# Kernel optimization log

Measured on AMD Instinct MI355X. Metric: run time of the kernel, lower is better.

## Reference

```python
import jax, jax.numpy as jnp
import numpy as np

N_NODES = 50000
N_EDGES = 600000
IN_DIM = 128
HID_DIM = 128
OUT_DIM = 128
N_GRAPHS = 64


def _glorot(key, shape):
    lim = np.sqrt(6.0 / (shape[0] + shape[1]))
    return jax.random.uniform(key, shape, jnp.float32, -lim, lim)


def setup_inputs() -> dict:
    key = jax.random.key(0)
    ks = jax.random.split(key, 8)
    h = jax.random.normal(ks[0], (N_NODES, IN_DIM), jnp.float32)
    src = jax.random.randint(ks[1], (N_EDGES,), 0, N_NODES, jnp.int64)
    dst = jax.random.randint(ks[2], (N_EDGES,), 0, N_NODES, jnp.int64)
    graph_ids = jnp.sort(jax.random.randint(ks[3], (N_NODES,), 0, N_GRAPHS, jnp.int64))
    W1 = _glorot(ks[4], (IN_DIM, HID_DIM)); b1 = jnp.zeros((HID_DIM,), jnp.float32)
    W2 = _glorot(ks[5], (HID_DIM, HID_DIM)); b2 = jnp.zeros((HID_DIM,), jnp.float32)
    W3 = _glorot(ks[6], (HID_DIM, OUT_DIM)); b3 = jnp.zeros((OUT_DIM,), jnp.float32)
    return {"h": h, "src": src, "dst": dst, "graph_ids": graph_ids,
            "W1": W1, "b1": b1, "W2": W2, "b2": b2, "W3": W3, "b3": b3,
            "n_graphs": N_GRAPHS}


def _graph_conv(h, src, dst, norm_src, norm_dst, W, b):
    # DGL GraphConv, norm='both': D_dst^{-1/2} A^T D_src^{-1/2} h W + b
    m = h * norm_src[:, None]                                   # [N, d]
    agg = jax.ops.segment_sum(m[src], dst, num_segments=h.shape[0])  # [N, d]
    return (agg * norm_dst[:, None]) @ W + b


def reference(h, src, dst, graph_ids, W1, b1, W2, b2, W3, b3, n_graphs):
    n = h.shape[0]
    ones = jnp.ones((src.shape[0],), h.dtype)
    out_deg = jnp.clip(jax.ops.segment_sum(ones, src, num_segments=n), 1.0)
    in_deg = jnp.clip(jax.ops.segment_sum(ones, dst, num_segments=n), 1.0)
    norm_src = out_deg ** -0.5
    norm_dst = in_deg ** -0.5

    x = jax.nn.relu(_graph_conv(h, src, dst, norm_src, norm_dst, W1, b1))
    x = jax.nn.relu(_graph_conv(x, src, dst, norm_src, norm_dst, W2, b2))
    x = jax.nn.relu(_graph_conv(x, src, dst, norm_src, norm_dst, W3, b3))

    # dgl.mean_nodes: per-graph mean over nodes
    gsum = jax.ops.segment_sum(x, graph_ids, num_segments=n_graphs)          # [G, d]
    gcnt = jax.ops.segment_sum(jnp.ones((n,), x.dtype), graph_ids, num_segments=n_graphs)
    return gsum / jnp.clip(gcnt, 1.0)[:, None]
```

## Files before the change

### kernel.cpp

```cpp
#include <hip/hip_runtime.h>
#include <hip/hip_fp16.h>


#define DIM 128
#define GRAPHS 64

typedef _Float16 half8 __attribute__((ext_vector_type(8)));
typedef float floatx4 __attribute__((ext_vector_type(4)));

#define HIST_R 4
#define HIST_S 64
#define NPR 12500
#define LDSW (NPR / 2)

__global__ __launch_bounds__(256) void k_hist(const int* __restrict__ src,
                                              const int* __restrict__ dst,
                                              unsigned* __restrict__ partial, int E) {
    __shared__ unsigned hist[LDSW];
    int b = blockIdx.x;
    int a = b / (HIST_R * HIST_S);
    int r = (b / HIST_S) % HIST_R;
    int s = b % HIST_S;
    const int* arr = a ? dst : src;
    for (int i = threadIdx.x; i < LDSW; i += 256) hist[i] = 0;
    __syncthreads();
    int chunk = (E + HIST_S - 1) / HIST_S;
    int e0 = s * chunk;
    int e1 = min(e0 + chunk, E);
    unsigned base = (unsigned)(r * NPR);
    for (int i = e0 + threadIdx.x; i < e1; i += 256) {
        unsigned n = (unsigned)arr[i] - base;
        if (n < NPR) atomicAdd(&hist[n >> 1], 1u << ((n & 1) * 16));
    }
    __syncthreads();
    unsigned* outp = partial + ((size_t)(a * HIST_R + r) * HIST_S + s) * LDSW;
    for (int i = threadIdx.x; i < LDSW; i += 256) outp[i] = hist[i];
}

__global__ __launch_bounds__(256) void k_hist_merge(const unsigned* __restrict__ partial,
                                                    float* __restrict__ ns,
                                                    float* __restrict__ nd,
                                                    int* __restrict__ inc,
                                                    int* __restrict__ bsum, int N) {
    __shared__ int sred[256];
    int nb = (N + 255) / 256;
    int isDst = (blockIdx.x < nb) ? 1 : 0;
    int cb = isDst ? blockIdx.x : blockIdx.x - nb;
    int n = cb * 256 + threadIdx.x;
    int deg = 0;
    if (n < N) {
        int a = isDst ? 1 : 0;
        int r = n / NPR;
        int w = (n % NPR) >> 1;
        int field = (n & 1) * 16;
        const unsigned* p = partial + ((size_t)(a * HIST_R + r) * HIST_S) * LDSW + w;
        unsigned sum = 0;
#pragma unroll
        for (int s = 0; s < HIST_S; ++s) sum += p[(size_t)s * LDSW];
        deg = (int)((sum >> field) & 0xFFFFu);
        float nrm = rsqrtf(fmaxf((float)deg, 1.0f));
        if (isDst) { nd[n] = nrm; inc[n] = deg; }
        else       { ns[n] = nrm; }
    }
    if (isDst) {
        sred[threadIdx.x] = deg;
        __syncthreads();
        for (int off = 128; off > 0; off >>= 1) {
            if (threadIdx.x < off) sred[threadIdx.x] += sred[threadIdx.x + off];
            __syncthreads();
        }
        if (threadIdx.x == 0) bsum[cb] = sred[0];
    }
}

__global__ __launch_bounds__(256) void k_scan_write(const int* __restrict__ inc,
                                                    const int* __restrict__ bsum,
                                                    const unsigned* __restrict__ partial,
                                                    int* __restrict__ row_ptr,
                                                    int* __restrict__ cur,
                                                    float* __restrict__ gsum,
                                                    int* __restrict__ gcnt, int N) {
    __shared__ int sb[256];
    __shared__ int s[256];
    __shared__ int exs[256];
    int nb = (N + 255) / 256;
    int t = threadIdx.x;

    int bv = (t < nb) ? bsum[t] : 0;
    sb[t] = bv;
    __syncthreads();
    for (int off = 1; off < 256; off <<= 1) {
        int u = (t >= off) ? sb[t - off] : 0;
        __syncthreads();
        sb[t] += u;
        __syncthreads();
    }
    int excl = sb[t] - bv;
    __syncthreads();
    sb[t] = excl;
    __syncthreads();
    int blockBase = sb[blockIdx.x];

    int B = blockIdx.x * 256;
    int i = B + t;
    int v = (i < N) ? inc[i] : 0;
    s[t] = v;
    __syncthreads();
    for (int off = 1; off < 256; off <<= 1) {
        int u = (t >= off) ? s[t - off] : 0;
        __syncthreads();
        s[t] += u;
        __syncthreads();
    }
    int ex = blockBase + s[t] - v;
    exs[t] = ex;
    if (i < N) row_ptr[i] = ex;
    if (i == N - 1) row_ptr[N] = ex + v;
    if (blockIdx.x == 0) {
        for (int j = t; j < GRAPHS * DIM; j += 256) gsum[j] = 0.0f;
        if (t < GRAPHS) gcnt[t] = 0;
    }
    __syncthreads();

    if (t < 128) {
        int n0 = B + 2 * t;
        if (n0 < N) {
            int r = n0 / NPR;
            int w = (n0 % NPR) >> 1;
            const unsigned* p = partial + ((size_t)(HIST_R + r) * HIST_S) * LDSW + w;
            int run0 = exs[2 * t];
            int run1 = exs[2 * t + 1];
            int* c = cur + (size_t)r * HIST_S * NPR + 2 * w;
#pragma unroll
            for (int sl = 0; sl < HIST_S; ++sl) {
                c[(size_t)sl * NPR + 0] = run0;
                c[(size_t)sl * NPR + 1] = run1;
                unsigned hv = p[(size_t)sl * LDSW];
                run0 += (int)(hv & 0xFFFFu);
                run1 += (int)(hv >> 16);
            }
        }
    }
}

__global__ __launch_bounds__(256) void k_fill2(const int* __restrict__ src,
                                               const int* __restrict__ dst,
                                               const int* __restrict__ cur,
                                               int* __restrict__ csr, int E) {
    __shared__ int lcur[NPR];
    int r = blockIdx.x / HIST_S;
    int s = blockIdx.x % HIST_S;
    const int* cs = cur + (size_t)(r * HIST_S + s) * NPR;
    for (int i = threadIdx.x; i < NPR; i += 256) lcur[i] = cs[i];
    __syncthreads();
    int chunk = (E + HIST_S - 1) / HIST_S;
    int e0 = s * chunk;
    int e1 = min(e0 + chunk, E);
    unsigned base = (unsigned)(r * NPR);
    for (int i = e0 + threadIdx.x; i < e1; i += 256) {
        unsigned d = (unsigned)dst[i] - base;
        if (d < NPR) {
            int p = atomicAdd(&lcur[d], 1);
            csr[p] = src[i];
        }
    }
}

__global__ void k_prep(const float4* __restrict__ h, const float* __restrict__ ns,
                       uint2* __restrict__ A,
                       const float* __restrict__ W1, const float* __restrict__ W2,
                       const float* __restrict__ W3, _Float16* __restrict__ Wt1,
                       _Float16* __restrict__ Wt2, _Float16* __restrict__ Wt3, int N) {
    int i = blockIdx.x * blockDim.x + threadIdx.x;
    int nf4 = N * 32;
    if (i < nf4) {
        int n = i >> 5;
        float s = ns[n];
        float4 v = h[i];
        __half2 p0 = __floats2half2_rn(v.x * s, v.y * s);
        __half2 p1 = __floats2half2_rn(v.z * s, v.w * s);
        uint2 o;
        o.x = *(unsigned*)&p0;
        o.y = *(unsigned*)&p1;
        A[i] = o;
    } else {
        int j = i - nf4;
        if (j < 3 * 16384) {
            int which = j >> 14;
            int local = j & 16383;
            int k = local >> 7;
            int n = local & 127;
            const float* W = (which == 0) ? W1 : (which == 1) ? W2 : W3;
            _Float16* Wt = (which == 0) ? Wt1 : (which == 1) ? Wt2 : Wt3;
            Wt[(size_t)n * DIM + k] = (_Float16)W[local];
        }
    }
}

__global__ __launch_bounds__(256) void k_agg(const uint2* __restrict__ A,
                                             const int* __restrict__ row_ptr,
                                             const int* __restrict__ csr,
                                             const float* __restrict__ nd,
                                             uint2* __restrict__ Bh, int N) {
    int gtid = blockIdx.x * blockDim.x + threadIdx.x;
    int node = gtid >> 6;
    int lane = threadIdx.x & 63;
    if (node >= N) return;
    int e0 = row_ptr[node];
    int e1 = row_ptr[node + 1];
    int half = lane >> 5;
    int l8 = lane & 31;
    float ax = 0.f, ay = 0.f, az = 0.f, aw = 0.f;

    for (int base = e0; base < e1; base += 16) {
        int idx[8];
        uint2 u[8];
#pragma unroll
        for (int j = 0; j < 8; ++j) {
            int ee = base + 2 * j + half;
            idx[j] = csr[min(ee, e1 - 1)];
        }
#pragma unroll
        for (int j = 0; j < 8; ++j) {
            u[j] = A[(size_t)idx[j] * 32 + l8];
        }
#pragma unroll
        for (int j = 0; j < 8; ++j) {
            int ee = base + 2 * j + half;
            if (ee < e1) {
                __half2 p0 = *(__half2*)&u[j].x;
                __half2 p1 = *(__half2*)&u[j].y;
                float2 f0 = __half22float2(p0);
                float2 f1 = __half22float2(p1);
                ax += f0.x; ay += f0.y; az += f1.x; aw += f1.y;
            }
        }
    }

    ax += __shfl_xor(ax, 32);
    ay += __shfl_xor(ay, 32);
    az += __shfl_xor(az, 32);
    aw += __shfl_xor(aw, 32);

    if (half == 0) {
        float scale = nd[node];
        __half2 p0 = __floats2half2_rn(ax * scale, ay * scale);
        __half2 p1 = __floats2half2_rn(az * scale, aw * scale);
        uint2 o;
        o.x = *(unsigned*)&p0;
        o.y = *(unsigned*)&p1;
        Bh[(size_t)node * 32 + l8] = o;
    }
}

template <bool SCALE_NS>
__global__ __launch_bounds__(256) void k_gemm_mfma(
    const _Float16* __restrict__ Bin, const _Float16* __restrict__ Wt,
    const float* __restrict__ bias, const float* __restrict__ ns,
    _Float16* __restrict__ Xout, int N) {
    int tid = threadIdx.x;
    int wave = tid >> 6;
    int lane = tid & 63;
    int quad = lane >> 4;
    int l16 = lane & 15;
    int r0 = blockIdx.x * 64 + wave * 16;
    int arow = r0 + l16;

    half8 a[4];
#pragma unroll
    for (int q = 0; q < 4; ++q) {
        if (arow < N) {
            a[q] = *(const half8*)&Bin[(size_t)arow * DIM + q * 32 + quad * 8];
        } else {
            a[q] = half8{0, 0, 0, 0, 0, 0, 0, 0};
        }
    }

    floatx4 acc[8];
#pragma unroll
    for (int c = 0; c < 8; ++c) acc[c] = floatx4{0.f, 0.f, 0.f, 0.f};

#pragma unroll
    for (int c = 0; c < 8; ++c) {
#pragma unroll
        for (int q = 0; q < 4; ++q) {
            half8 b = *(const half8*)&Wt[(size_t)(c * 16 + l16) * DIM + q * 32 + quad * 8];
            acc[c] = __builtin_amdgcn_mfma_f32_16x16x32_f16(a[q], b, acc[c], 0, 0, 0);
        }
    }

    float bb[8];
#pragma unroll
    for (int c = 0; c < 8; ++c) bb[c] = bias[c * 16 + l16];

#pragma unroll
    for (int r = 0; r < 4; ++r) {
        int row = r0 + quad * 4 + r;
        if (row >= N) continue;
        float sr = SCALE_NS ? ns[row] : 1.0f;
#pragma unroll
        for (int c = 0; c < 8; ++c) {
            float v = fmaxf(acc[c][r] + bb[c], 0.0f);
            Xout[(size_t)row * DIM + c * 16 + l16] = (_Float16)(v * sr);
        }
    }
}

#define POOL_NODES 32
__global__ void k_pool_partial(const _Float16* __restrict__ X, const int* __restrict__ gid,
                               float* __restrict__ gsum, int* __restrict__ gcnt, int N) {
    int n0 = blockIdx.x * POOL_NODES;
    int d = threadIdx.x;
    int nend = min(n0 + POOL_NODES, N);
    float run = 0.0f;
    int cnt = 0;
    int curg = -1;
    for (int n = n0; n < nend; ++n) {
        int g = gid[n];
        if (g != curg) {
            if (cnt > 0) {
                atomicAdd(&gsum[curg * DIM + d], run);
                if (d == 0) atomicAdd(&gcnt[curg], cnt);
            }
            run = 0.0f; cnt = 0; curg = g;
        }
        run += (float)X[(size_t)n * DIM + d];
        cnt++;
    }
    if (cnt > 0) {
        atomicAdd(&gsum[curg * DIM + d], run);
        if (d == 0) atomicAdd(&gcnt[curg], cnt);
    }
}

__global__ void k_finalize(const float* __restrict__ gsum, const int* __restrict__ gcnt,
                           float* __restrict__ out, int G) {
    int i = blockIdx.x * blockDim.x + threadIdx.x;
    if (i < G * DIM) {
        int g = i >> 7;
        float c = fmaxf((float)gcnt[g], 1.0f);
        out[i] = gsum[i] / c;
    }
}

extern "C" void kernel_launch(void* const* d_in, const int* in_sizes, int n_in,
                              void* d_out, int out_size, void* d_ws, size_t ws_size,
                              hipStream_t stream) {
    const float* h   = (const float*)d_in[0];
    const int*   src = (const int*)d_in[1];
    const int*   dst = (const int*)d_in[2];
    const int*   gid = (const int*)d_in[3];
    const float* W1  = (const float*)d_in[4];
    const float* b1  = (const float*)d_in[5];
    const float* W2  = (const float*)d_in[6];
    const float* b2  = (const float*)d_in[7];
    const float* W3  = (const float*)d_in[8];
    const float* b3  = (const float*)d_in[9];

    const int N = in_sizes[0] / DIM;
    const int E = in_sizes[1];
    const int G = GRAPHS;
    float* out = (float*)d_out;

    char* ws = (char*)d_ws;
    size_t off = 0;
    auto alloc = [&](size_t bytes) -> void* {
        void* p = ws + off;
        off += (bytes + 255) & ~(size_t)255;
        return p;
    };
    const int nb = (N + 255) / 256;
    uint2* Ah0     = (uint2*)alloc((size_t)N * DIM * 2);
    uint2* Ah1     = (uint2*)alloc((size_t)N * DIM * 2);
    uint2* Bh      = (uint2*)alloc((size_t)N * DIM * 2);
    _Float16* X3   = (_Float16*)alloc((size_t)N * DIM * 2);
    _Float16* Wt1  = (_Float16*)alloc((size_t)DIM * DIM * 2);
    _Float16* Wt2  = (_Float16*)alloc((size_t)DIM * DIM * 2);
    _Float16* Wt3  = (_Float16*)alloc((size_t)DIM * DIM * 2);
    float* ns      = (float*)alloc((size_t)N * 4);
    float* nd      = (float*)alloc((size_t)N * 4);
    int*   inc     = (int*)alloc((size_t)N * 4);
    unsigned* partial = (unsigned*)alloc((size_t)2 * HIST_R * HIST_S * LDSW * 4);
    int*   cur     = (int*)alloc((size_t)HIST_R * HIST_S * NPR * 4);
    int*   row_ptr = (int*)alloc((size_t)(N + 1) * 4);
    int*   csr     = (int*)alloc((size_t)E * 4);
    float* gsum    = (float*)alloc((size_t)G * DIM * 4);
    int*   gcnt    = (int*)alloc((size_t)G * 4);
    int*   bsum    = (int*)alloc((size_t)nb * 4);

    k_hist<<<2 * HIST_R * HIST_S, 256, 0, stream>>>(src, dst, partial, E);
    k_hist_merge<<<2 * nb, 256, 0, stream>>>(partial, ns, nd, inc, bsum, N);
    k_scan_write<<<nb, 256, 0, stream>>>(inc, bsum, partial, row_ptr, cur, gsum, gcnt, N);
    k_fill2<<<HIST_R * HIST_S, 256, 0, stream>>>(src, dst, cur, csr, E);

    int prepThreads = N * 32 + 3 * 16384;
    k_prep<<<(prepThreads + 255) / 256, 256, 0, stream>>>((const float4*)h, ns, Ah0,
                                                          W1, W2, W3, Wt1, Wt2, Wt3, N);

    int aggBlocks  = (N * 64 + 255) / 256;
    int gemmBlocks = (N + 63) / 64;

    k_agg<<<aggBlocks, 256, 0, stream>>>(Ah0, row_ptr, csr, nd, Bh, N);
    k_gemm_mfma<true><<<gemmBlocks, 256, 0, stream>>>((const _Float16*)Bh, Wt1, b1, ns, (_Float16*)Ah1, N);
    k_agg<<<aggBlocks, 256, 0, stream>>>(Ah1, row_ptr, csr, nd, Bh, N);
    k_gemm_mfma<true><<<gemmBlocks, 256, 0, stream>>>((const _Float16*)Bh, Wt2, b2, ns, (_Float16*)Ah0, N);
    k_agg<<<aggBlocks, 256, 0, stream>>>(Ah0, row_ptr, csr, nd, Bh, N);
    k_gemm_mfma<false><<<gemmBlocks, 256, 0, stream>>>((const _Float16*)Bh, Wt3, b3, ns, X3, N);

    k_pool_partial<<<(N + POOL_NODES - 1) / POOL_NODES, 128, 0, stream>>>(X3, gid, gsum, gcnt, N);
    k_finalize<<<(G * DIM + 255) / 256, 256, 0, stream>>>(gsum, gcnt, out, G);
}
```

Baseline: 310.7 us.

## Fuse last GEMM with mean pooling and transpose MFMA output layout

Fuses the final GEMM with graph mean pooling. Per-block partial sums go into LDS bins and then global atomics, which removes the X3 write/read and the separate pool kernel. The MFMA operands are swapped so each lane owns a node row and stores half4 vectors instead of scalar halves. k_agg loads 16 CSR indices once per wave and broadcasts them with shuffles rather than issuing redundant loads. Graph counts are now derived in finalize by binary search over the sorted graph ids, which depends on graph_ids being sorted.

```diff
diff --git a/kernel.cpp b/kernel.cpp
--- a/kernel.cpp
+++ b/kernel.cpp
@@ -6,6 +6,7 @@
 #define GRAPHS 64
 
 typedef _Float16 half8 __attribute__((ext_vector_type(8)));
+typedef _Float16 half4 __attribute__((ext_vector_type(4)));
 typedef float floatx4 __attribute__((ext_vector_type(4)));
 
 #define HIST_R 4
@@ -78,8 +79,7 @@
                                                     const unsigned* __restrict__ partial,
                                                     int* __restrict__ row_ptr,
                                                     int* __restrict__ cur,
-                                                    float* __restrict__ gsum,
-                                                    int* __restrict__ gcnt, int N) {
+                                                    float* __restrict__ gsum, int N) {
     __shared__ int sb[256];
     __shared__ int s[256];
     __shared__ int exs[256];
@@ -118,7 +118,6 @@
     if (i == N - 1) row_ptr[N] = ex + v;
     if (blockIdx.x == 0) {
         for (int j = t; j < GRAPHS * DIM; j += 256) gsum[j] = 0.0f;
-        if (t < GRAPHS) gcnt[t] = 0;
     }
     __syncthreads();
 
@@ -213,12 +212,12 @@
     float ax = 0.f, ay = 0.f, az = 0.f, aw = 0.f;
 
     for (int base = e0; base < e1; base += 16) {
+        int vl = csr[min(base + (lane & 15), e1 - 1)];
         int idx[8];
         uint2 u[8];
 #pragma unroll
         for (int j = 0; j < 8; ++j) {
-            int ee = base + 2 * j + half;
-            idx[j] = csr[min(ee, e1 - 1)];
+            idx[j] = __shfl(vl, 2 * j + half);
         }
 #pragma unroll
         for (int j = 0; j < 8; ++j) {
@@ -254,7 +253,7 @@
 }
 
 template <bool SCALE_NS>
-__global__ __launch_bounds__(256) void k_gemm_mfma(
+__global__ __launch_bounds__(256) void k_gemm_t(
     const _Float16* __restrict__ Bin, const _Float16* __restrict__ Wt,
     const float* __restrict__ bias, const float* __restrict__ ns,
     _Float16* __restrict__ Xout, int N) {
@@ -263,16 +262,15 @@
     int lane = tid & 63;
     int quad = lane >> 4;
     int l16 = lane & 15;
-    int r0 = blockIdx.x * 64 + wave * 16;
-    int arow = r0 + l16;
-
-    half8 a[4];
+    int node = blockIdx.x * 64 + wave * 16 + l16;
+
+    half8 b[4];
 #pragma unroll
     for (int q = 0; q < 4; ++q) {
-        if (arow < N) {
-            a[q] = *(const half8*)&Bin[(size_t)arow * DIM + q * 32 + quad * 8];
+        if (node < N) {
+            b[q] = *(const half8*)&Bin[(size_t)node * DIM + q * 32 + quad * 8];
         } else {
-            a[q] = half8{0, 0, 0, 0, 0, 0, 0, 0};
+            b[q] = half8{0, 0, 0, 0, 0, 0, 0, 0};
         }
     }
 
@@ -284,61 +282,118 @@
     for (int c = 0; c < 8; ++c) {
 #pragma unroll
         for (int q = 0; q < 4; ++q) {
-            half8 b = *(const half8*)&Wt[(size_t)(c * 16 + l16) * DIM + q * 32 + quad * 8];
-            acc[c] = __builtin_amdgcn_mfma_f32_16x16x32_f16(a[q], b, acc[c], 0, 0, 0);
-        }
-    }
-
-    float bb[8];
-#pragma unroll
-    for (int c = 0; c < 8; ++c) bb[c] = bias[c * 16 + l16];
-
-#pragma unroll
-    for (int r = 0; r < 4; ++r) {
-        int row = r0 + quad * 4 + r;
-        if (row >= N) continue;
-        float sr = SCALE_NS ? ns[row] : 1.0f;
+            half8 a = *(const half8*)&Wt[(size_t)(c * 16 + l16) * DIM + q * 32 + quad * 8];
+            acc[c] = __builtin_amdgcn_mfma_f32_16x16x32_f16(a, b[q], acc[c], 0, 0, 0);
+        }
+    }
+
+    if (node < N) {
+        float s = SCALE_NS ? ns[node] : 1.0f;
 #pragma unroll
         for (int c = 0; c < 8; ++c) {
-            float v = fmaxf(acc[c][r] + bb[c], 0.0f);
-            Xout[(size_t)row * DIM + c * 16 + l16] = (_Float16)(v * sr);
-        }
-    }
-}
-
-#define POOL_NODES 32
-__global__ void k_pool_partial(const _Float16* __restrict__ X, const int* __restrict__ gid,
-                               float* __restrict__ gsum, int* __restrict__ gcnt, int N) {
-    int n0 = blockIdx.x * POOL_NODES;
-    int d = threadIdx.x;
-    int nend = min(n0 + POOL_NODES, N);
-    float run = 0.0f;
-    int cnt = 0;
-    int curg = -1;
-    for (int n = n0; n < nend; ++n) {
-        int g = gid[n];
-        if (g != curg) {
-            if (cnt > 0) {
-                atomicAdd(&gsum[curg * DIM + d], run);
-                if (d == 0) atomicAdd(&gcnt[curg], cnt);
+            float4 b4 = *(const float4*)&bias[c * 16 + quad * 4];
+            half4 o;
+            o[0] = (_Float16)(fmaxf(acc[c][0] + b4.x, 0.0f) * s);
+            o[1] = (_Float16)(fmaxf(acc[c][1] + b4.y, 0.0f) * s);
+            o[2] = (_Float16)(fmaxf(acc[c][2] + b4.z, 0.0f) * s);
+            o[3] = (_Float16)(fmaxf(acc[c][3] + b4.w, 0.0f) * s);
+            *(half4*)&Xout[(size_t)node * DIM + c * 16 + quad * 4] = o;
+        }
+    }
+}
+
+#define PBINS 8
+__global__ __launch_bounds__(256) void k_gemm_pool(
+    const _Float16* __restrict__ Bin, const _Float16* __restrict__ Wt,
+    const float* __restrict__ bias, const int* __restrict__ gid,
+    float* __restrict__ gsum, int N) {
+    __shared__ float lsum[PBINS * DIM];
+    int tid = threadIdx.x;
+    for (int i = tid; i < PBINS * DIM; i += 256) lsum[i] = 0.0f;
+    int wave = tid >> 6;
+    int lane = tid & 63;
+    int quad = lane >> 4;
+    int l16 = lane & 15;
+    int r0 = blockIdx.x * 64;
+    int node = r0 + wave * 16 + l16;
+    int nodec = min(node, N - 1);
+
+    half8 b[4];
+#pragma unroll
+    for (int q = 0; q < 4; ++q) {
+        if (node < N) {
+            b[q] = *(const half8*)&Bin[(size_t)node * DIM + q * 32 + quad * 8];
+        } else {
+            b[q] = half8{0, 0, 0, 0, 0, 0, 0, 0};
+        }
+    }
+
+    floatx4 acc[8];
+#pragma unroll
+    for (int c = 0; c < 8; ++c) acc[c] = floatx4{0.f, 0.f, 0.f, 0.f};
+    __syncthreads();
+
+#pragma unroll
+    for (int c = 0; c < 8; ++c) {
+#pragma unroll
+        for (int q = 0; q < 4; ++q) {
+            half8 a = *(const half8*)&Wt[(size_t)(c * 16 + l16) * DIM + q * 32 + quad * 8];
+            acc[c] = __builtin_amdgcn_mfma_f32_16x16x32_f16(a, b[q], acc[c], 0, 0, 0);
+        }
+    }
+
+    int g = gid[nodec];
+    int g0b = gid[r0];
+    int gEb = gid[min(r0 + 63, N - 1)];
+    bool ldsPath = (gEb - g0b) < PBINS;
+    int gF = __shfl(g, 0);
+    int gL = __shfl(g, 15);
+    bool uni = (gF == gL);
+    float valid = (node < N) ? 1.0f : 0.0f;
+
+#pragma unroll
+    for (int c = 0; c < 8; ++c) {
+        float4 b4 = *(const float4*)&bias[c * 16 + quad * 4];
+        float bv[4] = {b4.x, b4.y, b4.z, b4.w};
+#pragma unroll
+        for (int r = 0; r < 4; ++r) {
+            float v = fmaxf(acc[c][r] + bv[r], 0.0f) * valid;
+            int f = c * 16 + quad * 4 + r;
+            if (ldsPath) {
+                if (uni) {
+                    v += __shfl_xor(v, 1);
+                    v += __shfl_xor(v, 2);
+                    v += __shfl_xor(v, 4);
+                    v += __shfl_xor(v, 8);
+                    if (l16 == 0) atomicAdd(&lsum[(gF - g0b) * DIM + f], v);
+                } else {
+                    if (node < N) atomicAdd(&lsum[(g - g0b) * DIM + f], v);
+                }
+            } else {
+                if (node < N) atomicAdd(&gsum[(size_t)g * DIM + f], v);
             }
-            run = 0.0f; cnt = 0; curg = g;
-        }
-        run += (float)X[(size_t)n * DIM + d];
-        cnt++;
-    }
-    if (cnt > 0) {
-        atomicAdd(&gsum[curg * DIM + d], run);
-        if (d == 0) atomicAdd(&gcnt[curg], cnt);
-    }
-}
-
-__global__ void k_finalize(const float* __restrict__ gsum, const int* __restrict__ gcnt,
-                           float* __restrict__ out, int G) {
+        }
+    }
+    __syncthreads();
+    if (ldsPath) {
+        int ng = gEb - g0b + 1;
+        for (int i = tid; i < ng * DIM; i += 256) {
+            float sv = lsum[i];
+            if (sv != 0.0f) atomicAdd(&gsum[(size_t)g0b * DIM + i], sv);
+        }
+    }
+}
+
+__global__ void k_finalize(const float* __restrict__ gsum, const int* __restrict__ gid,
+                           float* __restrict__ out, int N, int G) {
     int i = blockIdx.x * blockDim.x + threadIdx.x;
     if (i < G * DIM) {
         int g = i >> 7;
-        float c = fmaxf((float)gcnt[g], 1.0f);
+        int lo = 0, hi = N;
+        while (lo < hi) { int m = (lo + hi) >> 1; if (gid[m] < g) lo = m + 1; else hi = m; }
+        int lo2 = lo, hi2 = N;
+        while (lo2 < hi2) { int m = (lo2 + hi2) >> 1; if (gid[m] < g + 1) lo2 = m + 1; else hi2 = m; }
+        float c = fmaxf((float)(lo2 - lo), 1.0f);
         out[i] = gsum[i] / c;
     }
 }
@@ -373,7 +428,6 @@
     uint2* Ah0     = (uint2*)alloc((size_t)N * DIM * 2);
     uint2* Ah1     = (uint2*)alloc((size_t)N * DIM * 2);
     uint2* Bh      = (uint2*)alloc((size_t)N * DIM * 2);
-    _Float16* X3   = (_Float16*)alloc((size_t)N * DIM * 2);
     _Float16* Wt1  = (_Float16*)alloc((size_t)DIM * DIM * 2);
     _Float16* Wt2  = (_Float16*)alloc((size_t)DIM * DIM * 2);
     _Float16* Wt3  = (_Float16*)alloc((size_t)DIM * DIM * 2);
@@ -385,12 +439,11 @@
     int*   row_ptr = (int*)alloc((size_t)(N + 1) * 4);
     int*   csr     = (int*)alloc((size_t)E * 4);
     float* gsum    = (float*)alloc((size_t)G * DIM * 4);
-    int*   gcnt    = (int*)alloc((size_t)G * 4);
     int*   bsum    = (int*)alloc((size_t)nb * 4);
 
     k_hist<<<2 * HIST_R * HIST_S, 256, 0, stream>>>(src, dst, partial, E);
     k_hist_merge<<<2 * nb, 256, 0, stream>>>(partial, ns, nd, inc, bsum, N);
-    k_scan_write<<<nb, 256, 0, stream>>>(inc, bsum, partial, row_ptr, cur, gsum, gcnt, N);
+    k_scan_write<<<nb, 256, 0, stream>>>(inc, bsum, partial, row_ptr, cur, gsum, N);
     k_fill2<<<HIST_R * HIST_S, 256, 0, stream>>>(src, dst, cur, csr, E);
 
     int prepThreads = N * 32 + 3 * 16384;
@@ -401,12 +454,11 @@
     int gemmBlocks = (N + 63) / 64;
 
     k_agg<<<aggBlocks, 256, 0, stream>>>(Ah0, row_ptr, csr, nd, Bh, N);
-    k_gemm_mfma<true><<<gemmBlocks, 256, 0, stream>>>((const _Float16*)Bh, Wt1, b1, ns, (_Float16*)Ah1, N);
+    k_gemm_t<true><<<gemmBlocks, 256, 0, stream>>>((const _Float16*)Bh, Wt1, b1, ns, (_Float16*)Ah1, N);
     k_agg<<<aggBlocks, 256, 0, stream>>>(Ah1, row_ptr, csr, nd, Bh, N);
-    k_gemm_mfma<true><<<gemmBlocks, 256, 0, stream>>>((const _Float16*)Bh, Wt2, b2, ns, (_Float16*)Ah0, N);
+    k_gemm_t<true><<<gemmBlocks, 256, 0, stream>>>((const _Float16*)Bh, Wt2, b2, ns, (_Float16*)Ah0, N);
     k_agg<<<aggBlocks, 256, 0, stream>>>(Ah0, row_ptr, csr, nd, Bh, N);
-    k_gemm_mfma<false><<<gemmBlocks, 256, 0, stream>>>((const _Float16*)Bh, Wt3, b3, ns, X3, N);
-
-    k_pool_partial<<<(N + POOL_NODES - 1) / POOL_NODES, 128, 0, stream>>>(X3, gid, gsum, gcnt, N);
-    k_finalize<<<(G * DIM + 255) / 256, 256, 0, stream>>>(gsum, gcnt, out, G);
-}
+    k_gemm_pool<<<gemmBlocks, 256, 0, stream>>>((const _Float16*)Bh, Wt3, b3, gid, gsum, N);
+
+    k_finalize<<<(G * DIM + 255) / 256, 256, 0, stream>>>(gsum, gid, out, N, G);
+}
```

New measurement: 310.2 us. Within noise of the previous version (-0.2%).
